# Kernel optimization log

Hardware: AMD Instinct MI355X
Metric: run time of the kernel (lower is better)

Reference implementation:

```python
import jax, jax.numpy as jnp
import numpy as np

L = 7          # window side (odd)
A = 0.3        # weight of average term
B = 0.7        # weight of differential term


def mex_hat(d):
    grid = (np.mgrid[:d, :d] - d // 2) * 1.0
    eucl = np.sqrt((grid ** 2).sum(0)) / d
    return (eucl * np.exp(-eucl)).astype(np.float32)  # (d, d)


def setup_inputs() -> dict:
    key = jax.random.key(0)
    x = jax.random.normal(key, (64, 1, 512, 512), dtype=jnp.float32)
    kernel = jnp.asarray(mex_hat(L).reshape(-1))  # (L*L,), matches unfold row-major order
    return {"x": x, "kernel": kernel}


def reference(x, kernel):
    # x: [B,1,n,n], kernel: [L*L]
    n = x.shape[2]
    pad = L // 2
    xp = jnp.pad(x, ((0, 0), (0, 0), (pad, pad), (pad, pad)))  # zero pad, as F.unfold
    mean_acc = jnp.zeros_like(x)
    diff_acc = jnp.zeros_like(x)
    # fixed 49-offset loop replaces the im2col buffer; each shift is a view-slice
    for i in range(L):
        for j in range(L):
            s = jax.lax.dynamic_slice(xp, (0, 0, i, j), x.shape)
            mean_acc = mean_acc + s
            diff_acc = diff_acc + kernel[i * L + j] * jax.nn.relu(s - x)
    average_term = jnp.exp(-mean_acc / (L * L))              # [B,1,n,n]
    differential_term = diff_acc                             # [B,1,n,n]
    mask = A * average_term + B * differential_term
    mask = mask / jnp.sqrt(jnp.sum(mask ** 2))               # global L2 norm
    out = jnp.where(x > mask, x, jnp.zeros_like(x))
    return out, average_term, differential_term
```

## Files before the change

### kernel.cpp

```cpp
#include <hip/hip_runtime.h>
#include <stdint.h>

#define IMG 512
constexpr float A_W = 0.3f, B_W = 0.7f;

constexpr int TX = 256, TY = 8;
constexpr int SMW = 264;
constexpr int SMH = TY + 6;
constexpr int NBX = IMG / TX;
constexpr int NBY = IMG / TY;

#define W1  0.12383970f
#define W2  0.16507309f
#define W4  0.21470754f
#define W5  0.23209061f
#define W8  0.26975268f
#define W9  0.27918814f
#define W10 0.28754623f
#define W13 0.30773566f
#define W18 0.33061044f

__device__ constexpr float KW[7][7] = {
    { W18, W13, W10, W9,  W10, W13, W18 },
    { W13, W8,  W5,  W4,  W5,  W8,  W13 },
    { W10, W5,  W2,  W1,  W2,  W5,  W10 },
    { W9,  W4,  W1,  0.f, W1,  W4,  W9  },
    { W10, W5,  W2,  W1,  W2,  W5,  W10 },
    { W13, W8,  W5,  W4,  W5,  W8,  W13 },
    { W18, W13, W10, W9,  W10, W13, W18 },
};

constexpr float ksum_calc() {
    float s = 0.f;
    for (int i = 0; i < 7; ++i)
        for (int j = 0; j < 7; ++j) s += KW[i][j];
    return s;
}
constexpr float KSUM = ksum_calc();

__global__ __launch_bounds__(256) void li_pass1(
    const float* __restrict__ x,
    float* __restrict__ outMask,
    float* __restrict__ outAvg,
    float* __restrict__ outDiff,
    float* __restrict__ partials)
{
    __shared__ float sm[SMH * SMW];
    __shared__ float red[4];
    const int tid = threadIdx.x;

    const int bx = blockIdx.x, by = blockIdx.y, b = blockIdx.z;
    const size_t imgBase = (size_t)b * IMG * IMG;
    const int x0 = bx * TX, y0 = by * TY;

    for (int idx = tid; idx < SMH * (SMW / 4); idx += 256) {
        const int ly = idx / (SMW / 4);
        const int fx = idx - ly * (SMW / 4);
        const int gy  = y0 - 3 + ly;
        const int gxf = x0 - 4 + 4 * fx;
        float4 v = make_float4(0.f, 0.f, 0.f, 0.f);
        if ((unsigned)gy < IMG && (unsigned)gxf <= (IMG - 4))
            v = *reinterpret_cast<const float4*>(&x[imgBase + (size_t)gy * IMG + gxf]);
        *reinterpret_cast<float4*>(&sm[ly * SMW + 4 * fx]) = v;
    }
    __syncthreads();

    const int lane = tid & 63;
    const int r2   = (tid >> 6) * 2;
    const int c0   = lane * 4;

    float4 C0 = *reinterpret_cast<const float4*>(&sm[(r2 + 3) * SMW + c0 + 4]);
    float4 C1 = *reinterpret_cast<const float4*>(&sm[(r2 + 4) * SMW + c0 + 4]);
    const float C[2][4] = { { C0.x, C0.y, C0.z, C0.w },
                            { C1.x, C1.y, C1.z, C1.w } };

    float T[2][4]  = { {0.f,0.f,0.f,0.f}, {0.f,0.f,0.f,0.f} };
    float MN[2][4] = { {0.f,0.f,0.f,0.f}, {0.f,0.f,0.f,0.f} };

    #pragma unroll
    for (int j = 0; j < 8; ++j) {
        const float4* smrow = reinterpret_cast<const float4*>(&sm[(r2 + j) * SMW + c0]);
        const float4 a0 = smrow[0], a1 = smrow[1], a2 = smrow[2];
        const float s[12] = { a0.x, a0.y, a0.z, a0.w,
                              a1.x, a1.y, a1.z, a1.w,
                              a2.x, a2.y, a2.z, a2.w };
        float rs[4];
        rs[0] = ((s[1] + s[2]) + (s[3] + s[4])) + ((s[5] + s[6]) + s[7]);
        rs[1] = (rs[0] - s[1]) + s[8];
        rs[2] = (rs[1] - s[2]) + s[9];
        rs[3] = (rs[2] - s[3]) + s[10];

        #pragma unroll
        for (int k = 0; k < 2; ++k) {
            const int dy = j - k;
            if (dy >= 0 && dy < 7) {
                #pragma unroll
                for (int c = 0; c < 4; ++c) MN[k][c] += rs[c];
                #pragma unroll
                for (int dx = 0; dx < 7; ++dx) {
                    if (KW[dy][dx] != 0.f) {
                        #pragma unroll
                        for (int c = 0; c < 4; ++c)
                            T[k][c] = fmaf(KW[dy][dx],
                                           fmaxf(s[c + dx + 1], C[k][c]), T[k][c]);
                    }
                }
            }
        }
    }

    float local = 0.f;
    #pragma unroll
    for (int k = 0; k < 2; ++k) {
        float av[4], dv[4], mv[4];
        #pragma unroll
        for (int c = 0; c < 4; ++c) {
            av[c] = __expf(MN[k][c] * (-1.f / 49.f));
            dv[c] = fmaf(-KSUM, C[k][c], T[k][c]);
            mv[c] = fmaf(A_W, av[c], B_W * dv[c]);
            local = fmaf(mv[c], mv[c], local);
        }
        const size_t g = imgBase + (size_t)(y0 + r2 + k) * IMG + (x0 + c0);
        *reinterpret_cast<float4*>(&outAvg[g])  = make_float4(av[0], av[1], av[2], av[3]);
        *reinterpret_cast<float4*>(&outDiff[g]) = make_float4(dv[0], dv[1], dv[2], dv[3]);
        *reinterpret_cast<float4*>(&outMask[g]) = make_float4(mv[0], mv[1], mv[2], mv[3]);
    }

    float v = local;
    #pragma unroll
    for (int off = 32; off > 0; off >>= 1) v += __shfl_down(v, off);
    if ((tid & 63) == 0) red[tid >> 6] = v;
    __syncthreads();
    if (tid == 0) {
        size_t pb = ((size_t)b * gridDim.y + by) * gridDim.x + bx;
        partials[pb] = red[0] + red[1] + red[2] + red[3];
    }
}

__global__ __launch_bounds__(1024) void li_reduce(
    const float* __restrict__ partials, int n, float* __restrict__ total)
{
    __shared__ float red[16];
    int tid = threadIdx.x;
    float v = 0.f;
    for (int i = tid; i < n; i += 1024) v += partials[i];
    #pragma unroll
    for (int off = 32; off > 0; off >>= 1) v += __shfl_down(v, off);
    if ((tid & 63) == 0) red[tid >> 6] = v;
    __syncthreads();
    if (tid == 0) {
        float s = 0.f;
        #pragma unroll
        for (int i = 0; i < 16; ++i) s += red[i];
        *total = s;
    }
}

__global__ __launch_bounds__(256) void li_pass2(
    const float4* __restrict__ x, const float4* __restrict__ mask,
    float4* __restrict__ out, const float* __restrict__ total)
{
    const float inv = 1.0f / sqrtf(*total);
    int i = blockIdx.x * 256 + threadIdx.x;
    float4 xv = x[i];
    float4 mv = mask[i];
    float4 ov;
    ov.x = (xv.x > mv.x * inv) ? xv.x : 0.f;
    ov.y = (xv.y > mv.y * inv) ? xv.y : 0.f;
    ov.z = (xv.z > mv.z * inv) ? xv.z : 0.f;
    ov.w = (xv.w > mv.w * inv) ? xv.w : 0.f;
    out[i] = ov;
}

extern "C" void kernel_launch(void* const* d_in, const int* in_sizes, int n_in,
                              void* d_out, int out_size, void* d_ws, size_t ws_size,
                              hipStream_t stream)
{
    const float* x = (const float*)d_in[0];
    const int Nelem = in_sizes[0];
    const int batch = Nelem / (IMG * IMG);

    float* out     = (float*)d_out;
    float* outMask = out;
    float* outAvg  = out + (size_t)Nelem;
    float* outDiff = out + (size_t)2 * Nelem;

    float* partials = (float*)d_ws;
    const int nblocks = NBX * NBY * batch;
    float* total = partials + nblocks;

    dim3 g1(NBX, NBY, batch);
    li_pass1<<<g1, 256, 0, stream>>>(x, outMask, outAvg, outDiff, partials);
    li_reduce<<<1, 1024, 0, stream>>>(partials, nblocks, total);

    const int nvec = Nelem / 4;
    li_pass2<<<nvec / 256, 256, 0, stream>>>(
        (const float4*)x, (const float4*)outMask, (float4*)out, total);
}
```

Before: 315.1 us.

## Fuse partial reduction into pass2, use packed f32x2 math, and enlarge tiles

The separate single-block reduction kernel is removed. Each pass2 block now re-sums the per-tile partials before running a grid-stride threshold loop, which drops one kernel launch and its serialization point. The stencil's max/fma inner loop is rewritten with 2-wide float vectors so the compiler can emit packed FP32 instructions. The pass1 tile grows to 16 rows with 512 threads, which reduces halo reload overhead. The cost is that all 2048 pass2 blocks redundantly read the partials array.

```diff
diff --git a/kernel.cpp b/kernel.cpp
--- a/kernel.cpp
+++ b/kernel.cpp
@@ -4,11 +4,25 @@
 #define IMG 512
 constexpr float A_W = 0.3f, B_W = 0.7f;
 
-constexpr int TX = 256, TY = 8;
+constexpr int TX = 256, TY = 16;
 constexpr int SMW = 264;
 constexpr int SMH = TY + 6;
 constexpr int NBX = IMG / TX;
 constexpr int NBY = IMG / TY;
+
+typedef float f32x2 __attribute__((ext_vector_type(2)));
+
+#if __has_builtin(__builtin_elementwise_fma) && __has_builtin(__builtin_elementwise_max)
+__device__ __forceinline__ f32x2 pk_max(f32x2 a, f32x2 b) { return __builtin_elementwise_max(a, b); }
+__device__ __forceinline__ f32x2 pk_fma(f32x2 a, f32x2 b, f32x2 c) { return __builtin_elementwise_fma(a, b, c); }
+#else
+__device__ __forceinline__ f32x2 pk_max(f32x2 a, f32x2 b) {
+    f32x2 r; r.x = fmaxf(a.x, b.x); r.y = fmaxf(a.y, b.y); return r;
+}
+__device__ __forceinline__ f32x2 pk_fma(f32x2 a, f32x2 b, f32x2 c) {
+    f32x2 r; r.x = fmaf(a.x, b.x, c.x); r.y = fmaf(a.y, b.y, c.y); return r;
+}
+#endif
 
 #define W1  0.12383970f
 #define W2  0.16507309f
@@ -38,7 +52,7 @@
 }
 constexpr float KSUM = ksum_calc();
 
-__global__ __launch_bounds__(256) void li_pass1(
+__global__ __launch_bounds__(512) void li_pass1(
     const float* __restrict__ x,
     float* __restrict__ outMask,
     float* __restrict__ outAvg,
@@ -46,14 +60,14 @@
     float* __restrict__ partials)
 {
     __shared__ float sm[SMH * SMW];
-    __shared__ float red[4];
+    __shared__ float red[8];
     const int tid = threadIdx.x;
 
     const int bx = blockIdx.x, by = blockIdx.y, b = blockIdx.z;
     const size_t imgBase = (size_t)b * IMG * IMG;
     const int x0 = bx * TX, y0 = by * TY;
 
-    for (int idx = tid; idx < SMH * (SMW / 4); idx += 256) {
+    for (int idx = tid; idx < SMH * (SMW / 4); idx += 512) {
         const int ly = idx / (SMW / 4);
         const int fx = idx - ly * (SMW / 4);
         const int gy  = y0 - 3 + ly;
@@ -71,10 +85,12 @@
 
     float4 C0 = *reinterpret_cast<const float4*>(&sm[(r2 + 3) * SMW + c0 + 4]);
     float4 C1 = *reinterpret_cast<const float4*>(&sm[(r2 + 4) * SMW + c0 + 4]);
-    const float C[2][4] = { { C0.x, C0.y, C0.z, C0.w },
-                            { C1.x, C1.y, C1.z, C1.w } };
-
-    float T[2][4]  = { {0.f,0.f,0.f,0.f}, {0.f,0.f,0.f,0.f} };
+    const f32x2 C2[2][2] = { { {C0.x, C0.y}, {C0.z, C0.w} },
+                             { {C1.x, C1.y}, {C1.z, C1.w} } };
+    const float Cs[2][4] = { { C0.x, C0.y, C0.z, C0.w },
+                             { C1.x, C1.y, C1.z, C1.w } };
+
+    f32x2 T2[2][2] = { { {0.f,0.f}, {0.f,0.f} }, { {0.f,0.f}, {0.f,0.f} } };
     float MN[2][4] = { {0.f,0.f,0.f,0.f}, {0.f,0.f,0.f,0.f} };
 
     #pragma unroll
@@ -99,10 +115,11 @@
                 #pragma unroll
                 for (int dx = 0; dx < 7; ++dx) {
                     if (KW[dy][dx] != 0.f) {
-                        #pragma unroll
-                        for (int c = 0; c < 4; ++c)
-                            T[k][c] = fmaf(KW[dy][dx],
-                                           fmaxf(s[c + dx + 1], C[k][c]), T[k][c]);
+                        const f32x2 w = { KW[dy][dx], KW[dy][dx] };
+                        const f32x2 sv0 = { s[dx + 1], s[dx + 2] };
+                        const f32x2 sv1 = { s[dx + 3], s[dx + 4] };
+                        T2[k][0] = pk_fma(w, pk_max(sv0, C2[k][0]), T2[k][0]);
+                        T2[k][1] = pk_fma(w, pk_max(sv1, C2[k][1]), T2[k][1]);
                     }
                 }
             }
@@ -112,11 +129,12 @@
     float local = 0.f;
     #pragma unroll
     for (int k = 0; k < 2; ++k) {
+        const float Tk[4] = { T2[k][0].x, T2[k][0].y, T2[k][1].x, T2[k][1].y };
         float av[4], dv[4], mv[4];
         #pragma unroll
         for (int c = 0; c < 4; ++c) {
             av[c] = __expf(MN[k][c] * (-1.f / 49.f));
-            dv[c] = fmaf(-KSUM, C[k][c], T[k][c]);
+            dv[c] = fmaf(-KSUM, Cs[k][c], Tk[c]);
             mv[c] = fmaf(A_W, av[c], B_W * dv[c]);
             local = fmaf(mv[c], mv[c], local);
         }
@@ -132,44 +150,45 @@
     if ((tid & 63) == 0) red[tid >> 6] = v;
     __syncthreads();
     if (tid == 0) {
+        float s = 0.f;
+        #pragma unroll
+        for (int i = 0; i < 8; ++i) s += red[i];
         size_t pb = ((size_t)b * gridDim.y + by) * gridDim.x + bx;
-        partials[pb] = red[0] + red[1] + red[2] + red[3];
-    }
-}
-
-__global__ __launch_bounds__(1024) void li_reduce(
-    const float* __restrict__ partials, int n, float* __restrict__ total)
+        partials[pb] = s;
+    }
+}
+
+__global__ __launch_bounds__(256) void li_pass2(
+    const float* __restrict__ partials, int np,
+    const float4* __restrict__ x,
+    float4* __restrict__ out,
+    long nvec4)
 {
-    __shared__ float red[16];
-    int tid = threadIdx.x;
+    __shared__ float red[4];
+    __shared__ float tot_sm;
+    const int tid = threadIdx.x;
+
     float v = 0.f;
-    for (int i = tid; i < n; i += 1024) v += partials[i];
+    for (int i = tid; i < np; i += 256) v += partials[i];
     #pragma unroll
     for (int off = 32; off > 0; off >>= 1) v += __shfl_down(v, off);
     if ((tid & 63) == 0) red[tid >> 6] = v;
     __syncthreads();
-    if (tid == 0) {
-        float s = 0.f;
-        #pragma unroll
-        for (int i = 0; i < 16; ++i) s += red[i];
-        *total = s;
-    }
-}
-
-__global__ __launch_bounds__(256) void li_pass2(
-    const float4* __restrict__ x, const float4* __restrict__ mask,
-    float4* __restrict__ out, const float* __restrict__ total)
-{
-    const float inv = 1.0f / sqrtf(*total);
-    int i = blockIdx.x * 256 + threadIdx.x;
-    float4 xv = x[i];
-    float4 mv = mask[i];
-    float4 ov;
-    ov.x = (xv.x > mv.x * inv) ? xv.x : 0.f;
-    ov.y = (xv.y > mv.y * inv) ? xv.y : 0.f;
-    ov.z = (xv.z > mv.z * inv) ? xv.z : 0.f;
-    ov.w = (xv.w > mv.w * inv) ? xv.w : 0.f;
-    out[i] = ov;
+    if (tid == 0) tot_sm = red[0] + red[1] + red[2] + red[3];
+    __syncthreads();
+    const float inv = 1.0f / sqrtf(tot_sm);
+
+    const size_t stride = (size_t)gridDim.x * 256;
+    for (size_t i = (size_t)blockIdx.x * 256 + tid; i < (size_t)nvec4; i += stride) {
+        float4 xv = x[i];
+        float4 mv = out[i];
+        float4 ov;
+        ov.x = (xv.x > mv.x * inv) ? xv.x : 0.f;
+        ov.y = (xv.y > mv.y * inv) ? xv.y : 0.f;
+        ov.z = (xv.z > mv.z * inv) ? xv.z : 0.f;
+        ov.w = (xv.w > mv.w * inv) ? xv.w : 0.f;
+        out[i] = ov;
+    }
 }
 
 extern "C" void kernel_launch(void* const* d_in, const int* in_sizes, int n_in,
@@ -186,14 +205,12 @@
     float* outDiff = out + (size_t)2 * Nelem;
 
     float* partials = (float*)d_ws;
-    const int nblocks = NBX * NBY * batch;
-    float* total = partials + nblocks;
+    const int np = NBX * NBY * batch;
 
     dim3 g1(NBX, NBY, batch);
-    li_pass1<<<g1, 256, 0, stream>>>(x, outMask, outAvg, outDiff, partials);
-    li_reduce<<<1, 1024, 0, stream>>>(partials, nblocks, total);
-
-    const int nvec = Nelem / 4;
-    li_pass2<<<nvec / 256, 256, 0, stream>>>(
-        (const float4*)x, (const float4*)outMask, (float4*)out, total);
-}
+    li_pass1<<<g1, 512, 0, stream>>>(x, outMask, outAvg, outDiff, partials);
+
+    const long nvec4 = (long)Nelem / 4;
+    li_pass2<<<2048, 256, 0, stream>>>(
+        partials, np, (const float4*)x, (float4*)out, nvec4);
+}
```

New measurement: 312.8 us. No clear change (-0.7%).
